# Performance work log

Measured on AMD Instinct MI355X. Metric: run time of the kernel, lower is better.

## Reference

```python
import jax, jax.numpy as jnp
import numpy as np
from jax import lax

B, T, N, D = 16, 96, 512, 128
M, K, H = 1196, 8, 4
TAU_TIME = 2.0
KW = 12  # depthwise kernel size


def _l2norm(x, axis=-1, eps=1e-12):
    n = jnp.sqrt(jnp.sum(x * x, axis=axis, keepdims=True))
    return x / jnp.maximum(n, eps)


def setup_inputs() -> dict:
    key = jax.random.key(0)
    ks = jax.random.split(key, 20)
    hid = N * D
    inp = {
        'x_scalar': jax.random.normal(ks[0], (B, T, N), jnp.float32),
        'season_q': jax.random.randint(ks[1], (B,), 0, 4),
        'year_q': jax.random.uniform(ks[2], (B,), jnp.float32, 0.0, 10.0),
        # temporal encoder params
        'dw_w': jax.random.normal(ks[3], (N, 1, KW), jnp.float32) * 0.1,
        'dw_b': jnp.zeros((N,), jnp.float32),
        'pw_w': jax.random.normal(ks[4], (hid, N), jnp.float32) * 0.02,
        'pw_b': jnp.zeros((hid,), jnp.float32),
        'ln_g': jnp.ones((D,), jnp.float32),
        'ln_b': jnp.zeros((D,), jnp.float32),
        # multi-head attention params (torch MultiheadAttention layout)
        'in_proj_w': jax.random.normal(ks[5], (3 * D, D), jnp.float32) * 0.05,
        'in_proj_b': jnp.zeros((3 * D,), jnp.float32),
        'out_proj_w': jax.random.normal(ks[6], (D, D), jnp.float32) * 0.05,
        'out_proj_b': jnp.zeros((D,), jnp.float32),
        # final projection
        'proj_w': jax.random.normal(ks[7], (D, D), jnp.float32) * 0.05,
        'proj_b': jnp.zeros((D,), jnp.float32),
        # memory bank buffers (assume memory is full: count == M)
        'memory_bank': jax.random.normal(ks[8], (M, N, D), jnp.float32),
        'memory_seasons': jax.random.randint(ks[9], (M,), 0, 4),
        'memory_years': jax.random.uniform(ks[10], (M,), jnp.float32, 0.0, 10.0),
    }
    return inp


def _encoder(x_scalar, dw_w, dw_b, pw_w, pw_b, ln_g, ln_b):
    # x_scalar: [B,T,N] -> (with d_input=1) channels = N, layout [B,N,T]
    x = jnp.transpose(x_scalar, (0, 2, 1))
    # depthwise conv, groups=N, kernel=12, padding=6 -> length T+1
    x = lax.conv_general_dilated(x, dw_w, window_strides=(1,), padding=[(6, 6)],
                                 dimension_numbers=('NCH', 'OIH', 'NCH'),
                                 feature_group_count=N)
    x = jax.nn.gelu(x + dw_b[None, :, None], approximate=False)
    # pointwise 1x1 conv == GEMM over channels: [B, N*D, T+1]
    x = jnp.einsum('oi,bit->bot', pw_w, x) + pw_b[None, :, None]
    x = jax.nn.gelu(x, approximate=False)
    # adaptive avg pool to 1 == mean over time
    q = jnp.mean(x, axis=-1).reshape(B, N, D)
    # layernorm over last dim
    mu = jnp.mean(q, axis=-1, keepdims=True)
    var = jnp.mean((q - mu) ** 2, axis=-1, keepdims=True)
    return (q - mu) / jnp.sqrt(var + 1e-5) * ln_g + ln_b


def _retrieve(q, season_q, year_q, memory_bank, memory_seasons, memory_years):
    q_flat = _l2norm(q.reshape(B, -1))            # [B, N*D]
    mem_flat = _l2norm(memory_bank.reshape(M, -1))  # [M, N*D]
    sim = q_flat @ mem_flat.T                     # [B, M]
    season_mask = (season_q[:, None] == memory_seasons[None, :]).astype(sim.dtype)
    sim = sim * season_mask + (1.0 - season_mask) * (-10000.0)
    delta_year = jnp.abs(year_q[:, None] - memory_years[None, :])
    diversity = 1.0 - jnp.exp(-delta_year / TAU_TIME)  # gap_years == 0 path
    sim = sim * (0.5 + 0.5 * diversity)
    _, topk_idx = lax.top_k(sim, K)               # [B, K]
    return memory_bank[topk_idx]                  # [B, K, N, D]


def reference(x_scalar, season_q, year_q, dw_w, dw_b, pw_w, pw_b, ln_g, ln_b,
              in_proj_w, in_proj_b, out_proj_w, out_proj_b, proj_w, proj_b,
              memory_bank, memory_seasons, memory_years):
    q = _encoder(x_scalar, dw_w, dw_b, pw_w, pw_b, ln_g, ln_b)      # [B,N,D]
    retrieved = _retrieve(q, season_q, year_q, memory_bank, memory_seasons, memory_years)
    kv = jnp.transpose(retrieved, (0, 2, 1, 3))                      # [B,N,K,D]
    dh = D // H
    wq, wk, wv = in_proj_w[:D], in_proj_w[D:2 * D], in_proj_w[2 * D:]
    bq, bk, bv = in_proj_b[:D], in_proj_b[D:2 * D], in_proj_b[2 * D:]
    qh = (q @ wq.T + bq).reshape(B, N, H, dh)
    kh = (kv @ wk.T + bk).reshape(B, N, K, H, dh)
    vh = (kv @ wv.T + bv).reshape(B, N, K, H, dh)
    scores = jnp.einsum('bnhd,bnkhd->bnhk', qh, kh) / jnp.sqrt(jnp.asarray(dh, q.dtype))
    attn = jax.nn.softmax(scores, axis=-1)
    ctx = jnp.einsum('bnhk,bnkhd->bnhd', attn, vh).reshape(B, N, D)
    out = ctx @ out_proj_w.T + out_proj_b
    return (out @ proj_w.T + proj_b, q)
```

## Files before the change

### kernel.cpp

```cpp
#include <hip/hip_runtime.h>
#include <hip/hip_bf16.h>

#define BB_ 16
#define TT_ 96
#define NN 512
#define DD 128
#define MM 1196
#define KK 8
#define HID 65536
#define TP 97
#define TPAD 128

typedef __attribute__((ext_vector_type(8))) short short8v;
typedef __attribute__((ext_vector_type(4))) float f32x4;

__device__ __forceinline__ float gelu_exact(float x) {
    return 0.5f * x * (1.0f + erff(x * 0.70710678118654752f));
}
__device__ __forceinline__ unsigned rne16(float f) {
    unsigned u = __float_as_uint(f);
    return (u + 0x7fffu + ((u >> 16) & 1u)) >> 16;
}
__device__ __forceinline__ float bf2f(short s) {
    return __uint_as_float(((unsigned)(unsigned short)s) << 16);
}
__device__ __forceinline__ void split2(float x, short& hi, short& lo) {
    unsigned h = rne16(x);
    hi = (short)h;
    float hf = __uint_as_float(h << 16);
    lo = (short)rne16(x - hf);
}
__device__ __forceinline__ void gload_lds16(const void* g, void* l) {
    __builtin_amdgcn_global_load_lds((const __attribute__((address_space(1))) void*)g,
                                     (__attribute__((address_space(3))) void*)l, 16, 0, 0);
}
__device__ __forceinline__ short8v pack8(float4 a, float4 b) {
    short t[8];
    t[0] = (short)rne16(a.x); t[1] = (short)rne16(a.y);
    t[2] = (short)rne16(a.z); t[3] = (short)rne16(a.w);
    t[4] = (short)rne16(b.x); t[5] = (short)rne16(b.y);
    t[6] = (short)rne16(b.z); t[7] = (short)rne16(b.w);
    return *(short8v*)t;
}
__device__ __forceinline__ int swz32(int row) {
    return (row & 3) ^ ((row >> 2) & 3);
}
__device__ __forceinline__ void stage_tile_sw(const short* g, short* lds, int tid) {
    #pragma unroll
    for (int j = 0; j < 8; ++j) {
        int row = j * 16 + (tid >> 4);
        int csrc = (tid & 15) ^ (row & 7);
        gload_lds16(g + row * 128 + csrc * 8, lds + j * 2048 + tid * 8);
    }
}
__device__ __forceinline__ short8v frag_ld(const short* lds, int row, int kk, int lk) {
    return *(const short8v*)&lds[row * 128 + (((kk << 2) + lk) ^ (row & 7)) * 8];
}

__global__ __launch_bounds__(256) void k0_cvt2(const float* __restrict__ src,
                                               short* __restrict__ hi, short* __restrict__ lo) {
    size_t i = ((size_t)blockIdx.x * 256 + threadIdx.x) * 8;
    float4 a = *(const float4*)(src + i);
    float4 b = *(const float4*)(src + i + 4);
    short h[8], l[8];
    split2(a.x, h[0], l[0]); split2(a.y, h[1], l[1]);
    split2(a.z, h[2], l[2]); split2(a.w, h[3], l[3]);
    split2(b.x, h[4], l[4]); split2(b.y, h[5], l[5]);
    split2(b.z, h[6], l[6]); split2(b.w, h[7], l[7]);
    *(short8v*)(hi + i) = *(short8v*)h;
    *(short8v*)(lo + i) = *(short8v*)l;
}

__global__ __launch_bounds__(256) void k1_conv(const float* __restrict__ x,
                                               const float* __restrict__ dw_w,
                                               const float* __restrict__ dw_b,
                                               short* __restrict__ xh,
                                               short* __restrict__ xl) {
    int b = blockIdx.y, n0 = blockIdx.x * 64;
    __shared__ float xs[96][64];
    __shared__ float ws[64][12];
    __shared__ float bs[64];
    int tid = threadIdx.x;
    for (int j = tid; j < 96 * 64; j += 256) {
        int t = j / 64, n = j % 64;
        xs[t][n] = x[(size_t)(b * TT_ + t) * NN + n0 + n];
    }
    for (int j = tid; j < 64 * 12; j += 256) {
        int n = j / 12, k = j % 12;
        ws[n][k] = dw_w[(size_t)(n0 + n) * 12 + k];
    }
    if (tid < 64) bs[tid] = dw_b[n0 + tid];
    __syncthreads();
    int n = tid % 64, g = tid / 64;
    for (int t = g; t < TP; t += 4) {
        float acc = bs[n];
        #pragma unroll
        for (int k = 0; k < 12; ++k) {
            int ti = t - 6 + k;
            if (ti >= 0 && ti < 96) acc += xs[ti][n] * ws[n][k];
        }
        float v = gelu_exact(acc);
        short h, l;
        split2(v, h, l);
        size_t idx = ((size_t)b * TPAD + t) * NN + n0 + n;
        xh[idx] = h; xl[idx] = l;
    }
    for (int t = TP + g; t < TPAD; t += 4) {
        size_t idx = ((size_t)b * TPAD + t) * NN + n0 + n;
        xh[idx] = 0; xl[idx] = 0;
    }
}

template <bool PRE>
__global__ __launch_bounds__(256, 4) void k2_split(const float* __restrict__ pw_w,
                                                   const short* __restrict__ aH,
                                                   const short* __restrict__ aL,
                                                   const float* __restrict__ pw_b,
                                                   const short* __restrict__ bH,
                                                   const short* __restrict__ bL,
                                                   float* __restrict__ q_pre) {
    int wgid = blockIdx.x;
    int xcd = wgid & 7;
    int r = wgid >> 3;
    int b = r & 15;
    int o0 = (xcd * 64 + (r >> 4)) * 128;
    __shared__ short AsH[4096], AsL[4096], BsH[4096], BsL[4096];
    __shared__ float red[128][2];
    int tid = threadIdx.x;
    int l = tid & 63, w = tid >> 6;
    int wr = w >> 1, wc = w & 1;
    int lrow = l & 15, lk = l >> 4;
    const short* bHb = bH + (size_t)b * TPAD * NN;
    const short* bLb = bL + (size_t)b * TPAD * NN;

    f32x4 acc[4][4];
    #pragma unroll
    for (int m = 0; m < 4; ++m)
        #pragma unroll
        for (int n = 0; n < 4; ++n) acc[m][n] = (f32x4){0.f, 0.f, 0.f, 0.f};

    for (int it = 0; it < 16; ++it) {
        int k0 = it * 32;
        #pragma unroll
        for (int j = 0; j < 2; ++j) {
            int row = j * 64 + (tid >> 2);
            int c = tid & 3;
            int sc = c ^ swz32(row);
            int dofs = (j * 256 + tid) * 8;
            gload_lds16(bHb + (size_t)row * NN + k0 + sc * 8, &BsH[dofs]);
            gload_lds16(bLb + (size_t)row * NN + k0 + sc * 8, &BsL[dofs]);
            if constexpr (PRE) {
                gload_lds16(aH + (size_t)(o0 + row) * 512 + k0 + sc * 8, &AsH[dofs]);
                gload_lds16(aL + (size_t)(o0 + row) * 512 + k0 + sc * 8, &AsL[dofs]);
            } else {
                const float* src = pw_w + (size_t)(o0 + row) * 512 + k0 + c * 8;
                float4 v0 = *(const float4*)(src);
                float4 v1 = *(const float4*)(src + 4);
                short h[8], lo[8];
                split2(v0.x, h[0], lo[0]); split2(v0.y, h[1], lo[1]);
                split2(v0.z, h[2], lo[2]); split2(v0.w, h[3], lo[3]);
                split2(v1.x, h[4], lo[4]); split2(v1.y, h[5], lo[5]);
                split2(v1.z, h[6], lo[6]); split2(v1.w, h[7], lo[7]);
                int didx = row * 32 + (c ^ swz32(row)) * 8;
                *(short8v*)&AsH[didx] = *(short8v*)h;
                *(short8v*)&AsL[didx] = *(short8v*)lo;
            }
        }
        __syncthreads();
        short8v ah[4], al[4], bh[4], bl[4];
        #pragma unroll
        for (int m = 0; m < 4; ++m) {
            int row = wr * 64 + m * 16 + lrow;
            int idx = row * 32 + (lk ^ swz32(row)) * 8;
            ah[m] = *(const short8v*)&AsH[idx];
            al[m] = *(const short8v*)&AsL[idx];
        }
        #pragma unroll
        for (int n = 0; n < 4; ++n) {
            int row = wc * 64 + n * 16 + lrow;
            int idx = row * 32 + (lk ^ swz32(row)) * 8;
            bh[n] = *(const short8v*)&BsH[idx];
            bl[n] = *(const short8v*)&BsL[idx];
        }
        #pragma unroll
        for (int m = 0; m < 4; ++m)
            #pragma unroll
            for (int n = 0; n < 4; ++n) {
                acc[m][n] = __builtin_amdgcn_mfma_f32_16x16x32_bf16(ah[m], bh[n], acc[m][n], 0, 0, 0);
                acc[m][n] = __builtin_amdgcn_mfma_f32_16x16x32_bf16(ah[m], bl[n], acc[m][n], 0, 0, 0);
                acc[m][n] = __builtin_amdgcn_mfma_f32_16x16x32_bf16(al[m], bh[n], acc[m][n], 0, 0, 0);
            }
        __syncthreads();
    }
    #pragma unroll
    for (int m = 0; m < 4; ++m) {
        #pragma unroll
        for (int reg = 0; reg < 4; ++reg) {
            int o_loc = wr * 64 + m * 16 + lk * 4 + reg;
            float bias = pw_b[o0 + o_loc];
            float s = 0.f;
            #pragma unroll
            for (int n = 0; n < 4; ++n) {
                int t = wc * 64 + n * 16 + lrow;
                if (t < TP) s += gelu_exact(acc[m][n][reg] + bias);
            }
            s += __shfl_xor(s, 1, 64);
            s += __shfl_xor(s, 2, 64);
            s += __shfl_xor(s, 4, 64);
            s += __shfl_xor(s, 8, 64);
            if (lrow == 0) red[o_loc][wc] = s;
        }
    }
    __syncthreads();
    if (tid < 128)
        q_pre[(size_t)b * HID + o0 + tid] = (red[tid][0] + red[tid][1]) * (1.0f / 97.0f);
}

__global__ __launch_bounds__(256) void k3_ln(const float* __restrict__ q_pre,
                                             const float* __restrict__ g,
                                             const float* __restrict__ beta,
                                             float* __restrict__ qout) {
    int row = blockIdx.x * 4 + (threadIdx.x >> 6);
    int lane = threadIdx.x & 63;
    const float* src = q_pre + (size_t)row * 128;
    float v0 = src[lane], v1 = src[lane + 64];
    float s = v0 + v1;
    #pragma unroll
    for (int m = 32; m >= 1; m >>= 1) s += __shfl_xor(s, m, 64);
    float mu = s * (1.f / 128.f);
    float d0 = v0 - mu, d1 = v1 - mu;
    float vs = d0 * d0 + d1 * d1;
    #pragma unroll
    for (int m = 32; m >= 1; m >>= 1) vs += __shfl_xor(vs, m, 64);
    float rstd = rsqrtf(vs * (1.f / 128.f) + 1e-5f);
    qout[(size_t)row * 128 + lane] = d0 * rstd * g[lane] + beta[lane];
    qout[(size_t)row * 128 + lane + 64] = d1 * rstd * g[lane + 64] + beta[lane + 64];
}

__global__ __launch_bounds__(256) void k3b_qnorm(const float* __restrict__ q, float* __restrict__ qnorm) {
    int b = blockIdx.x;
    const float* src = q + (size_t)b * HID;
    float s = 0.f;
    for (int i = threadIdx.x * 4; i < HID; i += 256 * 4) {
        float4 v = *(const float4*)(src + i);
        s += v.x * v.x + v.y * v.y + v.z * v.z + v.w * v.w;
    }
    #pragma unroll
    for (int m = 32; m >= 1; m >>= 1) s += __shfl_xor(s, m, 64);
    __shared__ float red[4];
    if ((threadIdx.x & 63) == 0) red[threadIdx.x >> 6] = s;
    __syncthreads();
    if (threadIdx.x == 0) qnorm[b] = sqrtf(red[0] + red[1] + red[2] + red[3]);
}

__global__ __launch_bounds__(256) void k4_sim(const float* __restrict__ mem,
                                              const float* __restrict__ q,
                                              float* __restrict__ sim_part,
                                              float* __restrict__ nrm_part) {
    int m0 = blockIdx.x * 4;
    int isp = blockIdx.y;
    int tid = threadIdx.x;
    float acc[4][16];
    float nr[4] = {0.f, 0.f, 0.f, 0.f};
    #pragma unroll
    for (int a = 0; a < 4; ++a)
        #pragma unroll
        for (int c = 0; c < 16; ++c) acc[a][c] = 0.f;
    int ibase = isp * 16384;
    for (int it = 0; it < 16; ++it) {
        int i = ibase + (it * 256 + tid) * 4;
        float4 mv[4];
        #pragma unroll
        for (int a = 0; a < 4; ++a) {
            mv[a] = *(const float4*)(mem + (size_t)(m0 + a) * HID + i);
            nr[a] += mv[a].x * mv[a].x + mv[a].y * mv[a].y + mv[a].z * mv[a].z + mv[a].w * mv[a].w;
        }
        #pragma unroll
        for (int c = 0; c < 16; ++c) {
            float4 qv = *(const float4*)(q + (size_t)c * HID + i);
            #pragma unroll
            for (int a = 0; a < 4; ++a)
                acc[a][c] += mv[a].x * qv.x + mv[a].y * qv.y + mv[a].z * qv.z + mv[a].w * qv.w;
        }
    }
    __shared__ float red[4][68];
    int wv = tid >> 6, lane = tid & 63;
    #pragma unroll
    for (int a = 0; a < 4; ++a)
        for (int c = 0; c < 17; ++c) {
            float v = (c < 16) ? acc[a][c] : nr[a];
            #pragma unroll
            for (int m = 32; m >= 1; m >>= 1) v += __shfl_xor(v, m, 64);
            if (lane == 0) red[wv][a * 17 + c] = v;
        }
    __syncthreads();
    if (tid < 68) {
        float v = red[0][tid] + red[1][tid] + red[2][tid] + red[3][tid];
        int a = tid / 17, r = tid % 17;
        if (r < 16) sim_part[((size_t)isp * 16 + r) * MM + m0 + a] = v;
        else nrm_part[(size_t)isp * MM + m0 + a] = v;
    }
}

__global__ __launch_bounds__(256) void k5_topk(const float* __restrict__ sim_part,
                                               const float* __restrict__ nrm_part,
                                               const float* __restrict__ qnorm,
                                               const int* __restrict__ season_q,
                                               const float* __restrict__ year_q,
                                               const int* __restrict__ mem_season,
                                               const float* __restrict__ mem_year,
                                               int* __restrict__ topk) {
    int b = blockIdx.x;
    int tid = threadIdx.x;
    __shared__ float sadj[MM];
    float nq = fmaxf(qnorm[b], 1e-12f);
    int sq = season_q[b];
    float yq = year_q[b];
    for (int m = tid; m < MM; m += 256) {
        float dot = 0.f, ns = 0.f;
        #pragma unroll
        for (int p = 0; p < 4; ++p) {
            dot += sim_part[((size_t)p * 16 + b) * MM + m];
            ns += nrm_part[(size_t)p * MM + m];
        }
        float nm = fmaxf(sqrtf(ns), 1e-12f);
        float s = dot / (nq * nm);
        if (mem_season[m] != sq) s = -10000.0f;
        float dy = fabsf(yq - mem_year[m]);
        float dv = 1.0f - expf(-dy * 0.5f);
        s *= (0.5f + 0.5f * dv);
        sadj[m] = s;
    }
    __syncthreads();
    __shared__ float rv[4];
    __shared__ int ri[4];
    for (int it = 0; it < 8; ++it) {
        float bv = -INFINITY;
        int bi = -1;
        for (int m = tid; m < MM; m += 256) {
            float v = sadj[m];
            if (v > bv || (v == bv && bi >= 0 && m < bi)) { bv = v; bi = m; }
        }
        #pragma unroll
        for (int msk = 32; msk >= 1; msk >>= 1) {
            float ov = __shfl_xor(bv, msk, 64);
            int oi = __shfl_xor(bi, msk, 64);
            if (oi >= 0 && (ov > bv || (ov == bv && (bi < 0 || oi < bi)))) { bv = ov; bi = oi; }
        }
        int lane = tid & 63, wv = tid >> 6;
        if (lane == 0) { rv[wv] = bv; ri[wv] = bi; }
        __syncthreads();
        if (tid == 0) {
            float fv = rv[0]; int fi = ri[0];
            for (int w = 1; w < 4; ++w)
                if (ri[w] >= 0 && (rv[w] > fv || (rv[w] == fv && (fi < 0 || ri[w] < fi)))) { fv = rv[w]; fi = ri[w]; }
            topk[b * KK + it] = fi;
            sadj[fi] = -INFINITY;
        }
        __syncthreads();
    }
}

__global__ __launch_bounds__(256) void k6w(const float* __restrict__ in_w,
                                           const float* __restrict__ ow,
                                           const float* __restrict__ ob,
                                           const float* __restrict__ pw,
                                           const float* __restrict__ pb,
                                           short* __restrict__ WQKV16,
                                           short* __restrict__ WC16,
                                           float* __restrict__ BC) {
    __shared__ float ow_s[16384];
    int tid = threadIdx.x;
    for (int i = tid * 4; i < 16384; i += 1024)
        *(float4*)&ow_s[i] = *(const float4*)&ow[i];
    for (int i = tid * 8; i < 49152; i += 2048) {
        float4 a = *(const float4*)(in_w + i);
        float4 b = *(const float4*)(in_w + i + 4);
        *(short8v*)(WQKV16 + i) = pack8(a, b);
    }
    __syncthreads();
    int d = tid >> 1, j0 = (tid & 1) * 64;
    float accv[64];
    #pragma unroll
    for (int j = 0; j < 64; ++j) accv[j] = 0.f;
    for (int i = 0; i < 128; ++i) {
        float wv = pw[d * 128 + i];
        const float* orow = &ow_s[i * 128 + j0];
        #pragma unroll
        for (int j = 0; j < 64; ++j) accv[j] += wv * orow[j];
    }
    #pragma unroll
    for (int j = 0; j < 64; ++j) WC16[d * 128 + j0 + j] = (short)rne16(accv[j]);
    if (tid < 128) {
        float s = pb[tid];
        for (int i = 0; i < 128; ++i) s += pw[tid * 128 + i] * ob[i];
        BC[tid] = s;
    }
}

__global__ __launch_bounds__(256) void k6q(const float* __restrict__ q,
                                           const short* __restrict__ WQKV16,
                                           const float* __restrict__ in_b,
                                           short* __restrict__ QH16) {
    int b = blockIdx.y;
    int n0 = blockIdx.x * 128;
    __shared__ short As[16384], Ws[16384];
    int tid = threadIdx.x;
    int l = tid & 63, w = tid >> 6;
    int wr = w >> 1, wc = w & 1;
    int lrow = l & 15, lk = l >> 4;

    stage_tile_sw(WQKV16, Ws, tid);
    {
        int row = tid >> 1, half = tid & 1;
        const float* src = q + ((size_t)b * NN + n0 + row) * 128 + half * 64;
        #pragma unroll
        for (int cc = 0; cc < 8; ++cc) {
            float4 v0 = *(const float4*)(src + cc * 8);
            float4 v1 = *(const float4*)(src + cc * 8 + 4);
            int chunk = half * 8 + cc;
            *(short8v*)&As[row * 128 + (chunk ^ (row & 7)) * 8] = pack8(v0, v1);
        }
    }
    __syncthreads();
    f32x4 acc[4][4];
    #pragma unroll
    for (int m = 0; m < 4; ++m)
        #pragma unroll
        for (int n = 0; n < 4; ++n) acc[m][n] = (f32x4){0.f, 0.f, 0.f, 0.f};
    #pragma unroll
    for (int kk = 0; kk < 4; ++kk) {
        short8v a[4], bw[4];
        #pragma unroll
        for (int m = 0; m < 4; ++m) a[m] = frag_ld(As, wr * 64 + m * 16 + lrow, kk, lk);
        #pragma unroll
        for (int n = 0; n < 4; ++n) bw[n] = frag_ld(Ws, wc * 64 + n * 16 + lrow, kk, lk);
        #pragma unroll
        for (int m = 0; m < 4; ++m)
            #pragma unroll
            for (int n = 0; n < 4; ++n)
                acc[m][n] = __builtin_amdgcn_mfma_f32_16x16x32_bf16(a[m], bw[n], acc[m][n], 0, 0, 0);
    }
    #pragma unroll
    for (int m = 0; m < 4; ++m)
        #pragma unroll
        for (int n = 0; n < 4; ++n)
            #pragma unroll
            for (int reg = 0; reg < 4; ++reg) {
                int r = wr * 64 + m * 16 + lk * 4 + reg;
                int dco = wc * 64 + n * 16 + lrow;
                QH16[((size_t)b * NN + n0 + r) * 128 + dco] = (short)rne16(acc[m][n][reg] + in_b[dco]);
            }
}

__global__ __launch_bounds__(256) void k6kv(const float* __restrict__ mem,
                                            const int* __restrict__ topk,
                                            const short* __restrict__ WQKV16,
                                            const float* __restrict__ in_b,
                                            short* __restrict__ KH16,
                                            short* __restrict__ VH16) {
    int b = blockIdx.y;
    int n0 = blockIdx.x * 16;
    __shared__ short As[16384], WkS[16384], WvS[16384];
    __shared__ int idx_s[8];
    int tid = threadIdx.x;
    int l = tid & 63, w = tid >> 6;
    int wr = w >> 1, wc = w & 1;
    int lrow = l & 15, lk = l >> 4;
    if (tid < 8) idx_s[tid] = topk[b * 8 + tid];
    stage_tile_sw(WQKV16 + 16384, WkS, tid);
    stage_tile_sw(WQKV16 + 32768, WvS, tid);
    __syncthreads();
    {
        int row = tid >> 1, half = tid & 1;
        int n = n0 + (row >> 3), k = row & 7;
        const float* src = mem + (size_t)idx_s[k] * HID + (size_t)n * 128 + half * 64;
        #pragma unroll
        for (int cc = 0; cc < 8; ++cc) {
            float4 v0 = *(const float4*)(src + cc * 8);
            float4 v1 = *(const float4*)(src + cc * 8 + 4);
            int chunk = half * 8 + cc;
            *(short8v*)&As[row * 128 + (chunk ^ (row & 7)) * 8] = pack8(v0, v1);
        }
    }
    __syncthreads();
    f32x4 ak_[4][4], av_[4][4];
    #pragma unroll
    for (int m = 0; m < 4; ++m)
        #pragma unroll
        for (int n = 0; n < 4; ++n) {
            ak_[m][n] = (f32x4){0.f, 0.f, 0.f, 0.f};
            av_[m][n] = (f32x4){0.f, 0.f, 0.f, 0.f};
        }
    #pragma unroll
    for (int kk = 0; kk < 4; ++kk) {
        short8v a[4], bk[4], bv[4];
        #pragma unroll
        for (int m = 0; m < 4; ++m) a[m] = frag_ld(As, wr * 64 + m * 16 + lrow, kk, lk);
        #pragma unroll
        for (int n = 0; n < 4; ++n) {
            bk[n] = frag_ld(WkS, wc * 64 + n * 16 + lrow, kk, lk);
            bv[n] = frag_ld(WvS, wc * 64 + n * 16 + lrow, kk, lk);
        }
        #pragma unroll
        for (int m = 0; m < 4; ++m)
            #pragma unroll
            for (int n = 0; n < 4; ++n) {
                ak_[m][n] = __builtin_amdgcn_mfma_f32_16x16x32_bf16(a[m], bk[n], ak_[m][n], 0, 0, 0);
                av_[m][n] = __builtin_amdgcn_mfma_f32_16x16x32_bf16(a[m], bv[n], av_[m][n], 0, 0, 0);
            }
    }
    #pragma unroll
    for (int m = 0; m < 4; ++m)
        #pragma unroll
        for (int n = 0; n < 4; ++n)
            #pragma unroll
            for (int reg = 0; reg < 4; ++reg) {
                int r = wr * 64 + m * 16 + lk * 4 + reg;
                int dco = wc * 64 + n * 16 + lrow;
                int nl = r >> 3, k = r & 7;
                size_t o = (((size_t)b * NN + n0 + nl) * 8 + k) * 128 + dco;
                KH16[o] = (short)rne16(ak_[m][n][reg] + in_b[128 + dco]);
                VH16[o] = (short)rne16(av_[m][n][reg] + in_b[256 + dco]);
            }
}

__global__ __launch_bounds__(256) void k6s(const short* __restrict__ QH16,
                                           const short* __restrict__ KH16,
                                           const short* __restrict__ VH16,
                                           short* __restrict__ CTX16) {
    int b = blockIdx.y;
    int n = blockIdx.x * 8 + (threadIdx.x >> 5);
    int dh = threadIdx.x & 31;
    int d0 = dh * 4;
    size_t qbase = ((size_t)b * NN + n) * 128;
    size_t kvbase = qbase * 8;
    short4 q4 = *(const short4*)(QH16 + qbase + d0);
    float q0 = bf2f(q4.x), q1 = bf2f(q4.y), q2 = bf2f(q4.z), q3 = bf2f(q4.w);
    float sc[8];
    #pragma unroll
    for (int k = 0; k < 8; ++k) {
        short4 k4 = *(const short4*)(KH16 + kvbase + k * 128 + d0);
        float p = q0 * bf2f(k4.x) + q1 * bf2f(k4.y) + q2 * bf2f(k4.z) + q3 * bf2f(k4.w);
        p += __shfl_xor(p, 1, 32);
        p += __shfl_xor(p, 2, 32);
        p += __shfl_xor(p, 4, 32);
        sc[k] = p * 0.17677669529663687f;
    }
    float mx = sc[0];
    #pragma unroll
    for (int k = 1; k < 8; ++k) mx = fmaxf(mx, sc[k]);
    float den = 0.f;
    #pragma unroll
    for (int k = 0; k < 8; ++k) { sc[k] = expf(sc[k] - mx); den += sc[k]; }
    float inv = 1.0f / den;
    float c0 = 0.f, c1 = 0.f, c2 = 0.f, c3 = 0.f;
    #pragma unroll
    for (int k = 0; k < 8; ++k) {
        short4 v4 = *(const short4*)(VH16 + kvbase + k * 128 + d0);
        c0 += sc[k] * bf2f(v4.x);
        c1 += sc[k] * bf2f(v4.y);
        c2 += sc[k] * bf2f(v4.z);
        c3 += sc[k] * bf2f(v4.w);
    }
    short4 o4;
    o4.x = (short)rne16(c0 * inv);
    o4.y = (short)rne16(c1 * inv);
    o4.z = (short)rne16(c2 * inv);
    o4.w = (short)rne16(c3 * inv);
    *(short4*)(CTX16 + qbase + d0) = o4;
}

__global__ __launch_bounds__(256) void k6f(const short* __restrict__ CTX16,
                                           const short* __restrict__ WC16,
                                           const float* __restrict__ BC,
                                           float* __restrict__ out) {
    int r0 = blockIdx.x * 128;
    __shared__ short As[16384], Ws[16384];
    int tid = threadIdx.x;
    int l = tid & 63, w = tid >> 6;
    int wr = w >> 1, wc = w & 1;
    int lrow = l & 15, lk = l >> 4;
    stage_tile_sw(CTX16 + (size_t)r0 * 128, As, tid);
    stage_tile_sw(WC16, Ws, tid);
    __syncthreads();
    f32x4 acc[4][4];
    #pragma unroll
    for (int m = 0; m < 4; ++m)
        #pragma unroll
        for (int n = 0; n < 4; ++n) acc[m][n] = (f32x4){0.f, 0.f, 0.f, 0.f};
    #pragma unroll
    for (int kk = 0; kk < 4; ++kk) {
        short8v a[4], bw[4];
        #pragma unroll
        for (int m = 0; m < 4; ++m) a[m] = frag_ld(As, wr * 64 + m * 16 + lrow, kk, lk);
        #pragma unroll
        for (int n = 0; n < 4; ++n) bw[n] = frag_ld(Ws, wc * 64 + n * 16 + lrow, kk, lk);
        #pragma unroll
        for (int m = 0; m < 4; ++m)
            #pragma unroll
            for (int n = 0; n < 4; ++n)
                acc[m][n] = __builtin_amdgcn_mfma_f32_16x16x32_bf16(a[m], bw[n], acc[m][n], 0, 0, 0);
    }
    #pragma unroll
    for (int m = 0; m < 4; ++m)
        #pragma unroll
        for (int n = 0; n < 4; ++n)
            #pragma unroll
            for (int reg = 0; reg < 4; ++reg) {
                int r = wr * 64 + m * 16 + lk * 4 + reg;
                int dco = wc * 64 + n * 16 + lrow;
                out[(size_t)(r0 + r) * 128 + dco] = acc[m][n][reg] + BC[dco];
            }
}

__global__ __launch_bounds__(256) void k6_attn(const float* __restrict__ mem,
                                               const float* __restrict__ q,
                                               const int* __restrict__ topk,
                                               const float* __restrict__ in_w,
                                               const float* __restrict__ in_b,
                                               const float* __restrict__ ow,
                                               const float* __restrict__ ob,
                                               const float* __restrict__ pw,
                                               const float* __restrict__ pb,
                                               float* __restrict__ out) {
    int b = blockIdx.y;
    int n0 = blockIdx.x * 4;
    int tid = threadIdx.x;
    __shared__ float kv_s[4][8][128];
    __shared__ float kh_s[4][8][128];
    __shared__ float vh_s[4][8][128];
    __shared__ float qin_s[4][128];
    __shared__ float qh_s[4][128];
    __shared__ float ctx_s[4][128];
    __shared__ float o1_s[4][128];
    __shared__ int idx_s[8];
    if (tid < 8) idx_s[tid] = topk[b * 8 + tid];
    __syncthreads();
    for (int j = tid; j < 4 * 8 * 32; j += 256) {
        int n = j >> 8;
        int k = (j >> 5) & 7;
        int d4 = (j & 31) * 4;
        float4 v = *(const float4*)(mem + (size_t)idx_s[k] * HID + (size_t)(n0 + n) * 128 + d4);
        *(float4*)&kv_s[n][k][d4] = v;
    }
    for (int j = tid; j < 4 * 32; j += 256) {
        int n = j >> 5;
        int d4 = (j & 31) * 4;
        *(float4*)&qin_s[n][d4] = *(const float4*)(q + (size_t)(b * NN + n0 + n) * 128 + d4);
    }
    __syncthreads();
    {
        int d = tid & 127, half = tid >> 7;
        for (int n2 = 0; n2 < 2; ++n2) {
            int n = half * 2 + n2;
            float a = in_b[d];
            const float* wr = in_w + (size_t)d * 128;
            #pragma unroll
            for (int i = 0; i < 128; i += 4) {
                float4 w4 = *(const float4*)(wr + i);
                a += w4.x * qin_s[n][i] + w4.y * qin_s[n][i + 1] + w4.z * qin_s[n][i + 2] + w4.w * qin_s[n][i + 3];
            }
            qh_s[n][d] = a;
        }
    }
    {
        int d = tid & 127, layer = tid >> 7;
        float ak[16], av[16];
        #pragma unroll
        for (int p = 0; p < 16; ++p) { ak[p] = in_b[128 + d]; av[p] = in_b[256 + d]; }
        const float* wkr = in_w + (size_t)(128 + d) * 128;
        const float* wvr = in_w + (size_t)(256 + d) * 128;
        for (int i = 0; i < 128; i += 4) {
            float4 wk4 = *(const float4*)(wkr + i);
            float4 wv4 = *(const float4*)(wvr + i);
            #pragma unroll
            for (int p = 0; p < 16; ++p) {
                int pg = layer * 16 + p;
                int n = pg >> 3, k = pg & 7;
                float4 x4 = *(const float4*)&kv_s[n][k][i];
                ak[p] += wk4.x * x4.x + wk4.y * x4.y + wk4.z * x4.z + wk4.w * x4.w;
                av[p] += wv4.x * x4.x + wv4.y * x4.y + wv4.z * x4.z + wv4.w * x4.w;
            }
        }
        #pragma unroll
        for (int p = 0; p < 16; ++p) {
            int pg = layer * 16 + p;
            int n = pg >> 3, k = pg & 7;
            kh_s[n][k][d] = ak[p];
            vh_s[n][k][d] = av[p];
        }
    }
    __syncthreads();
    {
        int n = tid >> 6, lane = tid & 63;
        int dh = lane & 31, hh = lane >> 5;
        #pragma unroll
        for (int hp = 0; hp < 2; ++hp) {
            int h = hp * 2 + hh;
            int dd0 = h * 32 + dh;
            float qv = qh_s[n][dd0];
            float sc[8];
            #pragma unroll
            for (int k = 0; k < 8; ++k) {
                float p = qv * kh_s[n][k][dd0];
                #pragma unroll
                for (int msk = 16; msk >= 1; msk >>= 1) p += __shfl_xor(p, msk, 32);
                sc[k] = p * 0.17677669529663687f;
            }
            float mx = sc[0];
            #pragma unroll
            for (int k = 1; k < 8; ++k) mx = fmaxf(mx, sc[k]);
            float den = 0.f;
            #pragma unroll
            for (int k = 0; k < 8; ++k) { sc[k] = expf(sc[k] - mx); den += sc[k]; }
            float inv = 1.0f / den;
            float c = 0.f;
            #pragma unroll
            for (int k = 0; k < 8; ++k) c += sc[k] * vh_s[n][k][dd0];
            ctx_s[n][dd0] = c * inv;
        }
    }
    __syncthreads();
    {
        int d = tid & 127, half = tid >> 7;
        for (int n2 = 0; n2 < 2; ++n2) {
            int n = half * 2 + n2;
            float a = ob[d];
            const float* wr = ow + (size_t)d * 128;
            #pragma unroll
            for (int i = 0; i < 128; i += 4) {
                float4 w4 = *(const float4*)(wr + i);
                a += w4.x * ctx_s[n][i] + w4.y * ctx_s[n][i + 1] + w4.z * ctx_s[n][i + 2] + w4.w * ctx_s[n][i + 3];
            }
            o1_s[n][d] = a;
        }
    }
    __syncthreads();
    {
        int d = tid & 127, half = tid >> 7;
        for (int n2 = 0; n2 < 2; ++n2) {
            int n = half * 2 + n2;
            float a = pb[d];
            const float* wr = pw + (size_t)d * 128;
            #pragma unroll
            for (int i = 0; i < 128; i += 4) {
                float4 w4 = *(const float4*)(wr + i);
                a += w4.x * o1_s[n][i] + w4.y * o1_s[n][i + 1] + w4.z * o1_s[n][i + 2] + w4.w * o1_s[n][i + 3];
            }
            out[(size_t)(b * NN + n0 + n) * 128 + d] = a;
        }
    }
}

extern "C" void kernel_launch(void* const* d_in, const int* in_sizes, int n_in,
                              void* d_out, int out_size, void* d_ws, size_t ws_size,
                              hipStream_t stream) {
    const float* x_scalar   = (const float*)d_in[0];
    const int*   season_q   = (const int*)d_in[1];
    const float* year_q     = (const float*)d_in[2];
    const float* dw_w       = (const float*)d_in[3];
    const float* dw_b       = (const float*)d_in[4];
    const float* pw_w       = (const float*)d_in[5];
    const float* pw_b       = (const float*)d_in[6];
    const float* ln_g       = (const float*)d_in[7];
    const float* ln_bb      = (const float*)d_in[8];
    const float* in_proj_w  = (const float*)d_in[9];
    const float* in_proj_b  = (const float*)d_in[10];
    const float* out_proj_w = (const float*)d_in[11];
    const float* out_proj_b = (const float*)d_in[12];
    const float* proj_w     = (const float*)d_in[13];
    const float* proj_b     = (const float*)d_in[14];
    const float* memory_bank= (const float*)d_in[15];
    const int*   mem_season = (const int*)d_in[16];
    const float* mem_year   = (const float*)d_in[17];

    float* out_final = (float*)d_out;
    float* q_out = out_final + (size_t)BB_ * NN * DD;

    float* ws = (float*)d_ws;
    size_t off = 0;
    float* QPRE  = ws + off; off += 1048576;
    float* QNORM = ws + off; off += 16;
    float* NRMP  = ws + off; off += 4 * MM;
    float* SIMP  = ws + off; off += 64 * MM;
    int*   TOPK  = (int*)(ws + off); off += 128;
    short* XH    = (short*)(ws + off); off += 524288;
    short* XL    = (short*)(ws + off); off += 524288;
    short* AH    = (short*)(ws + off); off += 16777216;
    short* AL    = (short*)(ws + off); off += 16777216;
    bool use_pre = (ws_size >= off * 4);

    short* WQKV16 = AH;
    short* WC16   = AH + 49152;
    float* BC     = (float*)(AH + 65536);
    short* QH16   = AH + 66048;
    short* KH16   = QH16 + 1048576;
    short* VH16   = KH16 + 8388608;
    short* CTX16  = VH16 + 8388608;

    k1_conv<<<dim3(8, 16), 256, 0, stream>>>(x_scalar, dw_w, dw_b, XH, XL);
    if (use_pre) {
        k0_cvt2<<<16384, 256, 0, stream>>>(pw_w, AH, AL);
        k2_split<true><<<8192, 256, 0, stream>>>(pw_w, AH, AL, pw_b, XH, XL, QPRE);
    } else {
        k2_split<false><<<8192, 256, 0, stream>>>(pw_w, nullptr, nullptr, pw_b, XH, XL, QPRE);
    }
    k3_ln<<<2048, 256, 0, stream>>>(QPRE, ln_g, ln_bb, q_out);
    k3b_qnorm<<<16, 256, 0, stream>>>(q_out, QNORM);
    k4_sim<<<dim3(299, 4), 256, 0, stream>>>(memory_bank, q_out, SIMP, NRMP);
    k5_topk<<<16, 256, 0, stream>>>(SIMP, NRMP, QNORM, season_q, year_q, mem_season, mem_year, TOPK);
    if (use_pre) {
        k6w<<<1, 256, 0, stream>>>(in_proj_w, out_proj_w, out_proj_b, proj_w, proj_b, WQKV16, WC16, BC);
        k6q<<<dim3(4, 16), 256, 0, stream>>>(q_out, WQKV16, in_proj_b, QH16);
        k6kv<<<dim3(32, 16), 256, 0, stream>>>(memory_bank, TOPK, WQKV16, in_proj_b, KH16, VH16);
        k6s<<<dim3(64, 16), 256, 0, stream>>>(QH16, KH16, VH16, CTX16);
        k6f<<<64, 256, 0, stream>>>(CTX16, WC16, BC, out_final);
    } else {
        k6_attn<<<dim3(128, 16), 256, 0, stream>>>(memory_bank, q_out, TOPK, in_proj_w, in_proj_b,
                                                   out_proj_w, out_proj_b, proj_w, proj_b, out_final);
    }
}
```

Measured before the change: 697.2 us.

## Retile pointwise GEMM waves to skip padded time columns beyond 112

Changes the warp tiling of the split-bf16 pointwise GEMM from a 2x2 arrangement of 64x64 tiles to four waves each owning 32 output rows across all 112 time columns (7 n-tiles), so columns 112-127 of the padded 128-wide time axis are no longer loaded or multiplied. Because each wave now covers the whole time axis, the LDS cross-wave reduction and its barrier are replaced by direct float4 stores of the per-row means. The cost is a larger accumulator array per thread (14 vs 16 tiles, but a different register shape) and more B-fragment reads per A fragment.

```diff
diff --git a/kernel.cpp b/kernel.cpp
--- a/kernel.cpp
+++ b/kernel.cpp
@@ -125,19 +125,17 @@
     int b = r & 15;
     int o0 = (xcd * 64 + (r >> 4)) * 128;
     __shared__ short AsH[4096], AsL[4096], BsH[4096], BsL[4096];
-    __shared__ float red[128][2];
     int tid = threadIdx.x;
     int l = tid & 63, w = tid >> 6;
-    int wr = w >> 1, wc = w & 1;
     int lrow = l & 15, lk = l >> 4;
     const short* bHb = bH + (size_t)b * TPAD * NN;
     const short* bLb = bL + (size_t)b * TPAD * NN;
 
-    f32x4 acc[4][4];
-    #pragma unroll
-    for (int m = 0; m < 4; ++m)
-        #pragma unroll
-        for (int n = 0; n < 4; ++n) acc[m][n] = (f32x4){0.f, 0.f, 0.f, 0.f};
+    f32x4 acc[2][7];
+    #pragma unroll
+    for (int m = 0; m < 2; ++m)
+        #pragma unroll
+        for (int n = 0; n < 7; ++n) acc[m][n] = (f32x4){0.f, 0.f, 0.f, 0.f};
 
     for (int it = 0; it < 16; ++it) {
         int k0 = it * 32;
@@ -147,8 +145,10 @@
             int c = tid & 3;
             int sc = c ^ swz32(row);
             int dofs = (j * 256 + tid) * 8;
-            gload_lds16(bHb + (size_t)row * NN + k0 + sc * 8, &BsH[dofs]);
-            gload_lds16(bLb + (size_t)row * NN + k0 + sc * 8, &BsL[dofs]);
+            if (!(j == 1 && (tid >> 2) >= 48)) {
+                gload_lds16(bHb + (size_t)row * NN + k0 + sc * 8, &BsH[dofs]);
+                gload_lds16(bLb + (size_t)row * NN + k0 + sc * 8, &BsL[dofs]);
+            }
             if constexpr (PRE) {
                 gload_lds16(aH + (size_t)(o0 + row) * 512 + k0 + sc * 8, &AsH[dofs]);
                 gload_lds16(aL + (size_t)(o0 + row) * 512 + k0 + sc * 8, &AsL[dofs]);
@@ -167,53 +167,53 @@
             }
         }
         __syncthreads();
-        short8v ah[4], al[4], bh[4], bl[4];
-        #pragma unroll
-        for (int m = 0; m < 4; ++m) {
-            int row = wr * 64 + m * 16 + lrow;
+        short8v ah[2], al[2];
+        #pragma unroll
+        for (int m = 0; m < 2; ++m) {
+            int row = w * 32 + m * 16 + lrow;
             int idx = row * 32 + (lk ^ swz32(row)) * 8;
             ah[m] = *(const short8v*)&AsH[idx];
             al[m] = *(const short8v*)&AsL[idx];
         }
         #pragma unroll
-        for (int n = 0; n < 4; ++n) {
-            int row = wc * 64 + n * 16 + lrow;
+        for (int n = 0; n < 7; ++n) {
+            int row = n * 16 + lrow;
             int idx = row * 32 + (lk ^ swz32(row)) * 8;
-            bh[n] = *(const short8v*)&BsH[idx];
-            bl[n] = *(const short8v*)&BsL[idx];
-        }
-        #pragma unroll
-        for (int m = 0; m < 4; ++m)
-            #pragma unroll
-            for (int n = 0; n < 4; ++n) {
-                acc[m][n] = __builtin_amdgcn_mfma_f32_16x16x32_bf16(ah[m], bh[n], acc[m][n], 0, 0, 0);
-                acc[m][n] = __builtin_amdgcn_mfma_f32_16x16x32_bf16(ah[m], bl[n], acc[m][n], 0, 0, 0);
-                acc[m][n] = __builtin_amdgcn_mfma_f32_16x16x32_bf16(al[m], bh[n], acc[m][n], 0, 0, 0);
-            }
+            short8v bh = *(const short8v*)&BsH[idx];
+            short8v bl = *(const short8v*)&BsL[idx];
+            #pragma unroll
+            for (int m = 0; m < 2; ++m) {
+                acc[m][n] = __builtin_amdgcn_mfma_f32_16x16x32_bf16(ah[m], bh, acc[m][n], 0, 0, 0);
+                acc[m][n] = __builtin_amdgcn_mfma_f32_16x16x32_bf16(ah[m], bl, acc[m][n], 0, 0, 0);
+                acc[m][n] = __builtin_amdgcn_mfma_f32_16x16x32_bf16(al[m], bh, acc[m][n], 0, 0, 0);
+            }
+        }
         __syncthreads();
     }
     #pragma unroll
-    for (int m = 0; m < 4; ++m) {
+    for (int m = 0; m < 2; ++m) {
+        float s4[4];
         #pragma unroll
         for (int reg = 0; reg < 4; ++reg) {
-            int o_loc = wr * 64 + m * 16 + lk * 4 + reg;
+            int o_loc = w * 32 + m * 16 + lk * 4 + reg;
             float bias = pw_b[o0 + o_loc];
             float s = 0.f;
             #pragma unroll
-            for (int n = 0; n < 4; ++n) {
-                int t = wc * 64 + n * 16 + lrow;
+            for (int n = 0; n < 7; ++n) {
+                int t = n * 16 + lrow;
                 if (t < TP) s += gelu_exact(acc[m][n][reg] + bias);
             }
             s += __shfl_xor(s, 1, 64);
             s += __shfl_xor(s, 2, 64);
             s += __shfl_xor(s, 4, 64);
             s += __shfl_xor(s, 8, 64);
-            if (lrow == 0) red[o_loc][wc] = s;
-        }
-    }
-    __syncthreads();
-    if (tid < 128)
-        q_pre[(size_t)b * HID + o0 + tid] = (red[tid][0] + red[tid][1]) * (1.0f / 97.0f);
+            s4[reg] = s * (1.0f / 97.0f);
+        }
+        if (lrow == 0) {
+            int o_loc = w * 32 + m * 16 + lk * 4;
+            *(float4*)(q_pre + (size_t)b * HID + o0 + o_loc) = make_float4(s4[0], s4[1], s4[2], s4[3]);
+        }
+    }
 }
 
 __global__ __launch_bounds__(256) void k3_ln(const float* __restrict__ q_pre,
```

Result: faster. 659.3 us, median of 2 (-5.4%).
